# Kernel optimization log

Measured on AMD Instinct MI355X. Metric: run time of the kernel, lower is better.

## Reference

```python
import jax, jax.numpy as jnp
import numpy as np

B, T, C = 4, 2048, 2048
N_HEAD = 16
HEAD_DIM = C // N_HEAD  # 128
ROPE_BASE = 10000.0


def rope_cache(dim, seq_len, base=ROPE_BASE):
    inv_freq = 1.0 / (base ** (jnp.arange(0, dim, 2, dtype=jnp.float32) / dim))
    t = jnp.arange(seq_len, dtype=jnp.float32)
    freqs = jnp.outer(t, inv_freq)  # [T, dim//2]
    return jnp.cos(freqs), jnp.sin(freqs)


def apply_rope(q, k, cos, sin):
    # q, k: [B, H, T, D], interleaved-pair rotation
    q1, q2 = q[..., 0::2], q[..., 1::2]
    k1, k2 = k[..., 0::2], k[..., 1::2]
    c = cos[None, None, :, :]
    s = sin[None, None, :, :]
    q_rot = jnp.stack([q1 * c - q2 * s, q1 * s + q2 * c], axis=-1).reshape(q.shape)
    k_rot = jnp.stack([k1 * c - k2 * s, k1 * s + k2 * c], axis=-1).reshape(k.shape)
    return q_rot, k_rot


def setup_inputs() -> dict:
    key = jax.random.key(0)
    k1, k2, k3 = jax.random.split(key, 3)
    x = jax.random.normal(k1, (B, T, C), dtype=jnp.float32)
    W_attn = jax.random.normal(k2, (3 * C, C), dtype=jnp.float32) * (1.0 / np.sqrt(C))
    W_proj = jax.random.normal(k3, (C, C), dtype=jnp.float32) * (1.0 / np.sqrt(C))
    return {"x": x, "W_attn": W_attn, "W_proj": W_proj}


def reference(x, W_attn, W_proj):
    Bx, Tx, Cx = x.shape
    qkv = jnp.einsum('btc,fc->btf', x, W_attn)  # [B, T, 3C]
    q, k, v = jnp.split(qkv, 3, axis=-1)
    # [B, H, T, D]
    q = q.reshape(Bx, Tx, N_HEAD, HEAD_DIM).transpose(0, 2, 1, 3)
    k = k.reshape(Bx, Tx, N_HEAD, HEAD_DIM).transpose(0, 2, 1, 3)
    v = v.reshape(Bx, Tx, N_HEAD, HEAD_DIM).transpose(0, 2, 1, 3)
    cos, sin = rope_cache(HEAD_DIM, Tx)
    q, k = apply_rope(q, k, cos, sin)
    scale = 1.0 / np.sqrt(HEAD_DIM)
    scores = jnp.einsum('bhqd,bhkd->bhqk', q, k) * scale
    causal = jnp.tril(jnp.ones((Tx, Tx), dtype=bool))
    scores = jnp.where(causal[None, None, :, :], scores, jnp.finfo(scores.dtype).min)
    attn = jax.nn.softmax(scores, axis=-1)
    y = jnp.einsum('bhqk,bhkd->bhqd', attn, v)
    y = y.transpose(0, 2, 1, 3).reshape(Bx, Tx, Cx)
    return jnp.einsum('btc,fc->btf', y, W_proj)
```

## Files before the change

### kernel.cpp

```cpp
#include <hip/hip_runtime.h>
#include <stdint.h>

#define TT 2048
#define CC 2048
#define NHEAD 16
#define HD 128
#define NB 4
#define MTOT (NB*TT)
#define KD 2048
#define NT 32

typedef __attribute__((ext_vector_type(8))) short bf16x8;
typedef __attribute__((ext_vector_type(4))) float f32x4;

__device__ __forceinline__ unsigned short f2bf(float f) {
  unsigned u = __float_as_uint(f);
  u += 0x7FFF + ((u >> 16) & 1);
  return (unsigned short)(u >> 16);
}
__device__ __forceinline__ float bf2f(unsigned short h) {
  return __uint_as_float(((unsigned)h) << 16);
}

__device__ __forceinline__ void gl_lds16(const unsigned short* g, short* l) {
  __builtin_amdgcn_global_load_lds(
      (const __attribute__((address_space(1))) void*)(g),
      (__attribute__((address_space(3))) void*)(l), 16, 0, 0);
}

#define MFMA16(a, b, c) __builtin_amdgcn_mfma_f32_16x16x32_bf16((a), (b), (c), 0, 0, 0)

#define PRE_MFMA() do { \
  __builtin_amdgcn_s_barrier(); \
  asm volatile("s_waitcnt lgkmcnt(0)" ::: "memory"); \
  __builtin_amdgcn_s_setprio(1); \
} while(0)
#define POST_MFMA() do { \
  __builtin_amdgcn_s_setprio(0); \
  __builtin_amdgcn_s_barrier(); \
  __builtin_amdgcn_sched_barrier(0); \
} while(0)

__global__ void k_f2b(const float* __restrict__ in, unsigned short* __restrict__ out, int n4) {
  int i = blockIdx.x * 256 + threadIdx.x;
  if (i >= n4) return;
  float4 v = reinterpret_cast<const float4*>(in)[i];
  ushort4 o;
  o.x = f2bf(v.x); o.y = f2bf(v.y); o.z = f2bf(v.z); o.w = f2bf(v.w);
  reinterpret_cast<ushort4*>(out)[i] = o;
}

__global__ void k_rope_tab(float* __restrict__ tab) {
  int t = blockIdx.x, i = threadIdx.x;
  double inv = exp2(-(double)i * (13.287712379549449062 / 64.0));
  double ang = (double)t * inv;
  tab[(t*64 + i)*2 + 0] = (float)cos(ang);
  tab[(t*64 + i)*2 + 1] = (float)sin(ang);
}

__device__ __forceinline__ void gemm256_core(
    const unsigned short* __restrict__ Ag,
    const unsigned short* __restrict__ Bg,
    int m0, int n0, short* lds, f32x4 (&acc)[8][4])
{
  const int tid = threadIdx.x;
  const int wid = tid >> 6, lane = tid & 63;
  const int wm = wid >> 2, wn = wid & 3;
  const int r15 = lane & 15, hi4 = lane >> 4;
  const int srow = wid*8 + (lane >> 3);
  const int schunk = (lane & 7) ^ (lane >> 3);

  const f32x4 fz = {0.f, 0.f, 0.f, 0.f};
#pragma unroll
  for (int i = 0; i < 8; i++)
#pragma unroll
    for (int j = 0; j < 4; j++) acc[i][j] = fz;

  int aoff0[8];
#pragma unroll
  for (int mi = 0; mi < 8; mi++) {
    int row = wm*128 + mi*16 + r15;
    aoff0[mi] = row*64 + ((hi4 ^ (row & 7))*8);
  }
  int boff0[4];
#pragma unroll
  for (int ni = 0; ni < 4; ni++) {
    int row = wn*64 + ni*16 + r15;
    boff0[ni] = row*64 + ((hi4 ^ (row & 7))*8);
  }

#define STAGE(G, L, GROW0, KT) do { \
    gl_lds16((G) + (size_t)((GROW0) + srow)*KD + (KT) + schunk*8, (L) + wid*512); \
    gl_lds16((G) + (size_t)((GROW0) + 64 + srow)*KD + (KT) + schunk*8, (L) + 4096 + wid*512); \
  } while(0)

  STAGE(Ag, lds,                        m0,       0);
  STAGE(Ag, lds + 8192,                 m0 + 128, 0);
  STAGE(Bg, lds + 32768,                n0,       0);
  STAGE(Bg, lds + 32768 + 8192,         n0 + 128, 0);
  STAGE(Bg, lds + 32768 + 16384,        n0,       64);
  STAGE(Bg, lds + 32768 + 16384 + 8192, n0 + 128, 64);
  asm volatile("s_waitcnt vmcnt(4)" ::: "memory");
  __builtin_amdgcn_s_barrier();
  __builtin_amdgcn_sched_barrier(0);

#pragma unroll 1
  for (int t = 0; t < NT; t++) {
    const int db = t & 1;
    short* Ab = lds + db*16384;
    short* Bb = lds + 32768 + db*16384;
    short* An = lds + (db ^ 1)*16384;
    const int kt = t*64;
    const bool stA = (t < NT - 1);
    const bool stB = (t < NT - 2);

    bf16x8 a[8], b[4][2];
#pragma unroll
    for (int mi = 0; mi < 8; mi++)
      a[mi] = *reinterpret_cast<const bf16x8*>(Ab + aoff0[mi]);
#pragma unroll
    for (int ni = 0; ni < 4; ni++) {
      b[ni][0] = *reinterpret_cast<const bf16x8*>(Bb + boff0[ni]);
      b[ni][1] = *reinterpret_cast<const bf16x8*>(Bb + (boff0[ni] ^ 32));
    }
    if (stA) {
      STAGE(Ag, An,        m0,       kt + 64);
      STAGE(Ag, An + 8192, m0 + 128, kt + 64);
    }
    PRE_MFMA();
#pragma unroll
    for (int mi = 0; mi < 8; mi++)
#pragma unroll
      for (int ni = 0; ni < 4; ni++)
        acc[mi][ni] = MFMA16(a[mi], b[ni][0], acc[mi][ni]);
    POST_MFMA();

#pragma unroll
    for (int mi = 0; mi < 8; mi++)
      a[mi] = *reinterpret_cast<const bf16x8*>(Ab + (aoff0[mi] ^ 32));
    if (stB) {
      STAGE(Bg, Bb,        n0,       kt + 128);
      STAGE(Bg, Bb + 8192, n0 + 128, kt + 128);
    }
    if (t >= NT - 2) asm volatile("s_waitcnt vmcnt(0)" ::: "memory");
    else             asm volatile("s_waitcnt vmcnt(4)" ::: "memory");
    PRE_MFMA();
#pragma unroll
    for (int mi = 0; mi < 8; mi++)
#pragma unroll
      for (int ni = 0; ni < 4; ni++)
        acc[mi][ni] = MFMA16(a[mi], b[ni][1], acc[mi][ni]);
    POST_MFMA();
  }
#undef STAGE
}

__global__ __launch_bounds__(512, 2) void k_qkv(
    const unsigned short* __restrict__ xb,
    const unsigned short* __restrict__ wab,
    unsigned short* __restrict__ qr,
    unsigned short* __restrict__ kr,
    unsigned short* __restrict__ vt)
{
  __shared__ __align__(16) short lds[65536];
  f32x4 acc[8][4];
  int bid = blockIdx.x;
  int swz = (bid & 7)*96 + (bid >> 3);
  int m0 = (swz / 24)*256, n0 = (swz % 24)*256;
  gemm256_core(xb, wab, m0, n0, lds, acc);

  int tid = threadIdx.x, wid = tid >> 6, lane = tid & 63;
  int wm = wid >> 2, wn = wid & 3, r15 = lane & 15, hi4 = lane >> 4;
  int nw0 = n0 + wn*64;
  int which = nw0 >> 11;
  int h = (nw0 & 2047) >> 7;
#pragma unroll
  for (int mi = 0; mi < 8; mi++) {
    int m_base = m0 + wm*128 + mi*16 + hi4*4;
    int b = m_base >> 11;
    int t0 = m_base & (TT - 1);
#pragma unroll
    for (int ni = 0; ni < 4; ni++) {
      int d = (nw0 & 127) + ni*16 + r15;
      if (which == 2) {
        ushort4 pv;
        pv.x = f2bf(acc[mi][ni][0]); pv.y = f2bf(acc[mi][ni][1]);
        pv.z = f2bf(acc[mi][ni][2]); pv.w = f2bf(acc[mi][ni][3]);
        *reinterpret_cast<ushort4*>(vt + ((size_t)((b*NHEAD + h)*HD + d))*TT + t0) = pv;
      } else {
        unsigned short* dst = (which == 0) ? qr : kr;
        size_t base = ((size_t)(b*NHEAD + h)*TT + t0)*HD + d;
#pragma unroll
        for (int r = 0; r < 4; r++) dst[base + (size_t)r*HD] = f2bf(acc[mi][ni][r]);
      }
    }
  }
}

__global__ __launch_bounds__(512, 2) void k_proj(
    const unsigned short* __restrict__ yb,
    const unsigned short* __restrict__ wpb,
    float* __restrict__ out)
{
  __shared__ __align__(16) short lds[65536];
  f32x4 acc[8][4];
  int bid = blockIdx.x;
  int swz = (bid & 7)*32 + (bid >> 3);
  int m0 = (swz / 8)*256, n0 = (swz % 8)*256;
  gemm256_core(yb, wpb, m0, n0, lds, acc);

  int tid = threadIdx.x, wid = tid >> 6, lane = tid & 63;
  int wm = wid >> 2, wn = wid & 3, r15 = lane & 15, hi4 = lane >> 4;
  int nw0 = n0 + wn*64;
#pragma unroll
  for (int mi = 0; mi < 8; mi++) {
    int m = m0 + wm*128 + mi*16 + hi4*4;
#pragma unroll
    for (int ni = 0; ni < 4; ni++) {
      int n = nw0 + ni*16 + r15;
#pragma unroll
      for (int r = 0; r < 4; r++)
        out[(size_t)(m + r)*CC + n] = acc[mi][ni][r];
    }
  }
}

__global__ void k_rope_apply(unsigned int* __restrict__ q32, unsigned int* __restrict__ k32,
                             const float* __restrict__ tab) {
  int i = blockIdx.x * 256 + threadIdx.x;
  int ii = i & 63;
  int t = (i >> 6) & (TT - 1);
  float c = tab[(t*64 + ii)*2], s = tab[(t*64 + ii)*2 + 1];
  unsigned qv = q32[i];
  float q1 = bf2f((unsigned short)qv), q2 = bf2f((unsigned short)(qv >> 16));
  unsigned short lo = f2bf(q1*c - q2*s), hi = f2bf(q1*s + q2*c);
  q32[i] = (unsigned)lo | ((unsigned)hi << 16);
  unsigned kv = k32[i];
  float k1 = bf2f((unsigned short)kv), k2 = bf2f((unsigned short)(kv >> 16));
  lo = f2bf(k1*c - k2*s); hi = f2bf(k1*s + k2*c);
  k32[i] = (unsigned)lo | ((unsigned)hi << 16);
}

__global__ __launch_bounds__(256) void k_attn(
    const unsigned short* __restrict__ qr,
    const unsigned short* __restrict__ kr,
    const unsigned short* __restrict__ vt,
    unsigned short* __restrict__ yb)
{
  __shared__ short Ks[64*128];
  __shared__ short Vs[128*64];
  __shared__ short Pw[4*16*64];
  int bid = blockIdx.x;
  int bh = bid & 63, pr = bid >> 6;
  int tid = threadIdx.x, w = tid >> 6, lane = tid & 63;
  int r15 = lane & 15, hi4 = lane >> 4;
  const unsigned short* qg = qr + (size_t)bh*TT*HD;
  const unsigned short* kg = kr + (size_t)bh*TT*HD;
  const unsigned short* vg = vt + (size_t)bh*HD*TT;
  const f32x4 fz = {0.f,0.f,0.f,0.f};
  const float scale = 0.08838834764831845f;
  int b = bh >> 4, h = bh & 15;

#pragma unroll 1
  for (int ph = 0; ph < 2; ph++) {
    int qb = ph ? (31 - pr) : pr;
    int qlo = qb*64 + w*16;
    bf16x8 qf[4];
    {
      int qrow = qlo + r15;
#pragma unroll
      for (int kk = 0; kk < 4; kk++)
        qf[kk] = *reinterpret_cast<const bf16x8*>(qg + (size_t)qrow*HD + kk*32 + hi4*8);
    }
    f32x4 ao[8];
#pragma unroll
    for (int i = 0; i < 8; i++) ao[i] = fz;
    float mrow[4], lsum[4];
#pragma unroll
    for (int r = 0; r < 4; r++) { mrow[r] = -3.0e38f; lsum[r] = 0.f; }
    int ntiles = qb + 1;
    for (int it = 0; it < ntiles; ++it) {
      int kv0 = it*64;
      __syncthreads();
#pragma unroll
      for (int i = 0; i < 4; i++) {
        int chunk = tid + i*256;
        int row = chunk >> 4, c16 = chunk & 15;
        uint4 v = *reinterpret_cast<const uint4*>(kg + (size_t)(kv0 + row)*HD + c16*8);
        *reinterpret_cast<uint4*>((char*)Ks + row*256 + ((c16 ^ (row & 7))*16)) = v;
      }
#pragma unroll
      for (int i = 0; i < 4; i++) {
        int chunk = tid + i*256;
        int d = chunk >> 3, c8 = chunk & 7;
        uint4 v = *reinterpret_cast<const uint4*>(vg + (size_t)d*TT + kv0 + c8*8);
        *reinterpret_cast<uint4*>((char*)Vs + d*128 + ((c8 ^ (d & 7))*16)) = v;
      }
      __syncthreads();
      f32x4 sacc[4];
#pragma unroll
      for (int n = 0; n < 4; n++) {
        sacc[n] = fz;
#pragma unroll
        for (int kk = 0; kk < 4; kk++) {
          int kvr = n*16 + r15;
          int ch = (kk*4 + hi4) ^ (kvr & 7);
          bf16x8 kf = *reinterpret_cast<const bf16x8*>((char*)Ks + kvr*256 + ch*16);
          sacc[n] = MFMA16(qf[kk], kf, sacc[n]);
        }
      }
      float p[4][4], rmax[4];
#pragma unroll
      for (int r = 0; r < 4; r++) {
        int qgi = qlo + hi4*4 + r;
        float mx = -3.0e38f;
#pragma unroll
        for (int n = 0; n < 4; n++) {
          int kvg = kv0 + n*16 + r15;
          float sv = sacc[n][r]*scale;
          sv = (kvg <= qgi) ? sv : -3.0e38f;
          p[n][r] = sv;
          mx = fmaxf(mx, sv);
        }
        rmax[r] = mx;
      }
#pragma unroll
      for (int mm = 1; mm < 16; mm <<= 1)
#pragma unroll
        for (int r = 0; r < 4; r++) rmax[r] = fmaxf(rmax[r], __shfl_xor(rmax[r], mm));
      float alpha[4], rsum[4];
#pragma unroll
      for (int r = 0; r < 4; r++) {
        float mnew = fmaxf(mrow[r], rmax[r]);
        alpha[r] = __expf(mrow[r] - mnew);
        mrow[r] = mnew;
        float sum = 0.f;
#pragma unroll
        for (int n = 0; n < 4; n++) {
          float pv = __expf(p[n][r] - mnew);
          p[n][r] = pv;
          sum += pv;
        }
        rsum[r] = sum;
      }
#pragma unroll
      for (int mm = 1; mm < 16; mm <<= 1)
#pragma unroll
        for (int r = 0; r < 4; r++) rsum[r] += __shfl_xor(rsum[r], mm);
#pragma unroll
      for (int r = 0; r < 4; r++) lsum[r] = lsum[r]*alpha[r] + rsum[r];
#pragma unroll
      for (int i = 0; i < 8; i++)
#pragma unroll
        for (int r = 0; r < 4; r++) ao[i][r] *= alpha[r];
#pragma unroll
      for (int r = 0; r < 4; r++) {
        int prow = hi4*4 + r;
#pragma unroll
        for (int n = 0; n < 4; n++) {
          int col = n*16 + r15;
          Pw[w*1024 + prow*64 + (col ^ ((prow & 7) << 3))] = (short)f2bf(p[n][r]);
        }
      }
#pragma unroll
      for (int kk = 0; kk < 2; kk++) {
        int prow = r15;
        int ch = (kk*4 + hi4) ^ (prow & 7);
        bf16x8 pa = *reinterpret_cast<const bf16x8*>((char*)(Pw + w*1024) + prow*128 + ch*16);
#pragma unroll
        for (int ds_ = 0; ds_ < 8; ds_++) {
          int d = ds_*16 + r15;
          int vch = (kk*4 + hi4) ^ (d & 7);
          bf16x8 vf = *reinterpret_cast<const bf16x8*>((char*)Vs + d*128 + vch*16);
          ao[ds_] = MFMA16(pa, vf, ao[ds_]);
        }
      }
    }
#pragma unroll
    for (int r = 0; r < 4; r++) {
      int t = qlo + hi4*4 + r;
      float inv = 1.f / lsum[r];
      size_t base = ((size_t)b*TT + t)*CC + h*HD + r15;
#pragma unroll
      for (int ds_ = 0; ds_ < 8; ds_++)
        yb[base + ds_*16] = f2bf(ao[ds_][r] * inv);
    }
  }
}

extern "C" void kernel_launch(void* const* d_in, const int* in_sizes, int n_in,
                              void* d_out, int out_size, void* d_ws, size_t ws_size,
                              hipStream_t stream) {
  const float* x  = (const float*)d_in[0];
  const float* wa = (const float*)d_in[1];
  const float* wp = (const float*)d_in[2];
  float* out = (float*)d_out;
  char* ws = (char*)d_ws;
  size_t off = 0;
  unsigned short* xb  = (unsigned short*)(ws + off); off += (size_t)MTOT*CC*2;
  unsigned short* wab = (unsigned short*)(ws + off); off += (size_t)3*CC*CC*2;
  unsigned short* wpb = (unsigned short*)(ws + off); off += (size_t)CC*CC*2;
  unsigned short* qr  = (unsigned short*)(ws + off); off += (size_t)MTOT*CC*2;
  unsigned short* kr  = (unsigned short*)(ws + off); off += (size_t)MTOT*CC*2;
  unsigned short* vt  = (unsigned short*)(ws + off); off += (size_t)MTOT*CC*2;
  unsigned short* yb  = (unsigned short*)(ws + off); off += (size_t)MTOT*CC*2;
  float* tab          = (float*)(ws + off);          off += (size_t)TT*64*2*4;

  k_f2b<<<dim3(16384), dim3(256), 0, stream>>>(x,  xb,  MTOT*CC/4);
  k_f2b<<<dim3(12288), dim3(256), 0, stream>>>(wa, wab, 3*CC*CC/4);
  k_f2b<<<dim3(4096),  dim3(256), 0, stream>>>(wp, wpb, CC*CC/4);
  k_rope_tab<<<dim3(TT), dim3(64), 0, stream>>>(tab);
  k_qkv<<<dim3(768), dim3(512), 0, stream>>>(xb, wab, qr, kr, vt);
  k_rope_apply<<<dim3(32768), dim3(256), 0, stream>>>((unsigned int*)qr, (unsigned int*)kr, tab);
  k_attn<<<dim3(1024), dim3(256), 0, stream>>>(qr, kr, vt, yb);
  k_proj<<<dim3(256), dim3(512), 0, stream>>>(yb, wpb, out);
}
```

Before: 494.6 us.

## Process two 64-row query blocks per wave with prefetched K/V and lazy rescaling

The attention kernel now gives each block 128 query rows, with each wave holding two 16-row Q fragments. Each K/V tile loaded into LDS is reused across twice as many queries, and the grid is halved. The next K/V tile is prefetched into registers while the current tile is computed, and the online softmax skips the accumulator rescale when no row max grows by more than 8. This cuts global K/V traffic and barriers per query, at the cost of more registers, lower occupancy and coarser causal load balancing.

```diff
diff --git a/kernel.cpp b/kernel.cpp
--- a/kernel.cpp
+++ b/kernel.cpp
@@ -249,7 +249,7 @@
 {
   __shared__ short Ks[64*128];
   __shared__ short Vs[128*64];
-  __shared__ short Pw[4*16*64];
+  __shared__ short Pw[4*32*64];
   int bid = blockIdx.x;
   int bh = bid & 63, pr = bid >> 6;
   int tid = threadIdx.x, w = tid >> 6, lane = tid & 63;
@@ -261,129 +261,251 @@
   const float scale = 0.08838834764831845f;
   int b = bh >> 4, h = bh & 15;
 
+  int kdst[4], vdst[4], ksoff[4];
+  size_t vsoff[4];
+#pragma unroll
+  for (int i = 0; i < 4; i++) {
+    int chunk = tid + i*256;
+    int row = chunk >> 4, c16 = chunk & 15;
+    kdst[i] = row*256 + ((c16 ^ (row & 7))*16);
+    ksoff[i] = row*HD + c16*8;
+    int d = chunk >> 3, c8 = chunk & 7;
+    vdst[i] = d*128 + ((c8 ^ (d & 7))*16);
+    vsoff[i] = (size_t)d*TT + c8*8;
+  }
+
 #pragma unroll 1
   for (int ph = 0; ph < 2; ph++) {
-    int qb = ph ? (31 - pr) : pr;
-    int qlo = qb*64 + w*16;
-    bf16x8 qf[4];
+    int qb = ph ? (15 - pr) : pr;
+    int qlo0 = qb*128 + w*16, qlo1 = qlo0 + 64;
+    bf16x8 qf0[4], qf1[4];
     {
-      int qrow = qlo + r15;
-#pragma unroll
-      for (int kk = 0; kk < 4; kk++)
-        qf[kk] = *reinterpret_cast<const bf16x8*>(qg + (size_t)qrow*HD + kk*32 + hi4*8);
-    }
-    f32x4 ao[8];
-#pragma unroll
-    for (int i = 0; i < 8; i++) ao[i] = fz;
-    float mrow[4], lsum[4];
-#pragma unroll
-    for (int r = 0; r < 4; r++) { mrow[r] = -3.0e38f; lsum[r] = 0.f; }
-    int ntiles = qb + 1;
+      int q0 = qlo0 + r15, q1 = qlo1 + r15;
+#pragma unroll
+      for (int kk = 0; kk < 4; kk++) {
+        qf0[kk] = *reinterpret_cast<const bf16x8*>(qg + (size_t)q0*HD + kk*32 + hi4*8);
+        qf1[kk] = *reinterpret_cast<const bf16x8*>(qg + (size_t)q1*HD + kk*32 + hi4*8);
+      }
+    }
+    f32x4 ao0[8], ao1[8];
+#pragma unroll
+    for (int i = 0; i < 8; i++) { ao0[i] = fz; ao1[i] = fz; }
+    float mrow0[4], lsum0[4], mrow1[4], lsum1[4];
+#pragma unroll
+    for (int r = 0; r < 4; r++) {
+      mrow0[r] = -3.0e38f; lsum0[r] = 0.f;
+      mrow1[r] = -3.0e38f; lsum1[r] = 0.f;
+    }
+    int ntiles = 2*qb + 2;
+    uint4 st[8];
+
+#pragma unroll
+    for (int i = 0; i < 4; i++) {
+      st[i]     = *reinterpret_cast<const uint4*>(kg + ksoff[i]);
+      st[4 + i] = *reinterpret_cast<const uint4*>(vg + vsoff[i]);
+    }
+    __syncthreads();
+#pragma unroll
+    for (int i = 0; i < 4; i++) {
+      *reinterpret_cast<uint4*>((char*)Ks + kdst[i]) = st[i];
+      *reinterpret_cast<uint4*>((char*)Vs + vdst[i]) = st[4 + i];
+    }
+    __syncthreads();
+
+#pragma unroll 1
     for (int it = 0; it < ntiles; ++it) {
       int kv0 = it*64;
-      __syncthreads();
-#pragma unroll
-      for (int i = 0; i < 4; i++) {
-        int chunk = tid + i*256;
-        int row = chunk >> 4, c16 = chunk & 15;
-        uint4 v = *reinterpret_cast<const uint4*>(kg + (size_t)(kv0 + row)*HD + c16*8);
-        *reinterpret_cast<uint4*>((char*)Ks + row*256 + ((c16 ^ (row & 7))*16)) = v;
-      }
-#pragma unroll
-      for (int i = 0; i < 4; i++) {
-        int chunk = tid + i*256;
-        int d = chunk >> 3, c8 = chunk & 7;
-        uint4 v = *reinterpret_cast<const uint4*>(vg + (size_t)d*TT + kv0 + c8*8);
-        *reinterpret_cast<uint4*>((char*)Vs + d*128 + ((c8 ^ (d & 7))*16)) = v;
-      }
-      __syncthreads();
-      f32x4 sacc[4];
+      bool more = (it + 1 < ntiles);
+      f32x4 s0[4], s1[4];
 #pragma unroll
       for (int n = 0; n < 4; n++) {
-        sacc[n] = fz;
+        s0[n] = fz; s1[n] = fz;
 #pragma unroll
         for (int kk = 0; kk < 4; kk++) {
           int kvr = n*16 + r15;
           int ch = (kk*4 + hi4) ^ (kvr & 7);
           bf16x8 kf = *reinterpret_cast<const bf16x8*>((char*)Ks + kvr*256 + ch*16);
-          sacc[n] = MFMA16(qf[kk], kf, sacc[n]);
-        }
-      }
-      float p[4][4], rmax[4];
-#pragma unroll
-      for (int r = 0; r < 4; r++) {
-        int qgi = qlo + hi4*4 + r;
-        float mx = -3.0e38f;
-#pragma unroll
-        for (int n = 0; n < 4; n++) {
-          int kvg = kv0 + n*16 + r15;
-          float sv = sacc[n][r]*scale;
-          sv = (kvg <= qgi) ? sv : -3.0e38f;
-          p[n][r] = sv;
-          mx = fmaxf(mx, sv);
-        }
-        rmax[r] = mx;
-      }
-#pragma unroll
-      for (int mm = 1; mm < 16; mm <<= 1)
-#pragma unroll
-        for (int r = 0; r < 4; r++) rmax[r] = fmaxf(rmax[r], __shfl_xor(rmax[r], mm));
-      float alpha[4], rsum[4];
-#pragma unroll
-      for (int r = 0; r < 4; r++) {
-        float mnew = fmaxf(mrow[r], rmax[r]);
-        alpha[r] = __expf(mrow[r] - mnew);
-        mrow[r] = mnew;
-        float sum = 0.f;
-#pragma unroll
-        for (int n = 0; n < 4; n++) {
-          float pv = __expf(p[n][r] - mnew);
-          p[n][r] = pv;
-          sum += pv;
-        }
-        rsum[r] = sum;
-      }
-#pragma unroll
-      for (int mm = 1; mm < 16; mm <<= 1)
-#pragma unroll
-        for (int r = 0; r < 4; r++) rsum[r] += __shfl_xor(rsum[r], mm);
-#pragma unroll
-      for (int r = 0; r < 4; r++) lsum[r] = lsum[r]*alpha[r] + rsum[r];
-#pragma unroll
-      for (int i = 0; i < 8; i++)
-#pragma unroll
-        for (int r = 0; r < 4; r++) ao[i][r] *= alpha[r];
-#pragma unroll
-      for (int r = 0; r < 4; r++) {
-        int prow = hi4*4 + r;
-#pragma unroll
-        for (int n = 0; n < 4; n++) {
-          int col = n*16 + r15;
-          Pw[w*1024 + prow*64 + (col ^ ((prow & 7) << 3))] = (short)f2bf(p[n][r]);
+          s1[n] = MFMA16(qf1[kk], kf, s1[n]);
+          s0[n] = MFMA16(qf0[kk], kf, s0[n]);
+        }
+      }
+      if (more) {
+        int nkv = kv0 + 64;
+#pragma unroll
+        for (int i = 0; i < 4; i++) {
+          st[i]     = *reinterpret_cast<const uint4*>(kg + (size_t)nkv*HD + ksoff[i]);
+          st[4 + i] = *reinterpret_cast<const uint4*>(vg + vsoff[i] + nkv);
+        }
+      }
+      {
+        float p[4][4], rmax[4];
+#pragma unroll
+        for (int r = 0; r < 4; r++) {
+          int qgi = qlo0 + hi4*4 + r;
+          float mx = -3.0e38f;
+#pragma unroll
+          for (int n = 0; n < 4; n++) {
+            int kvg = kv0 + n*16 + r15;
+            float sv = s0[n][r]*scale;
+            sv = (kvg <= qgi) ? sv : -3.0e38f;
+            p[n][r] = sv;
+            mx = fmaxf(mx, sv);
+          }
+          rmax[r] = mx;
+        }
+#pragma unroll
+        for (int mm = 1; mm < 16; mm <<= 1)
+#pragma unroll
+          for (int r = 0; r < 4; r++) rmax[r] = fmaxf(rmax[r], __shfl_xor(rmax[r], mm));
+        bool ng = (rmax[0] <= mrow0[0] + 8.f) && (rmax[1] <= mrow0[1] + 8.f)
+               && (rmax[2] <= mrow0[2] + 8.f) && (rmax[3] <= mrow0[3] + 8.f);
+        bool defer = __all(ng);
+        float alpha[4];
+#pragma unroll
+        for (int r = 0; r < 4; r++) {
+          if (defer) { alpha[r] = 1.f; }
+          else {
+            float mnew = fmaxf(mrow0[r], rmax[r]);
+            alpha[r] = __expf(mrow0[r] - mnew);
+            mrow0[r] = mnew;
+          }
+        }
+        float rsum[4];
+#pragma unroll
+        for (int r = 0; r < 4; r++) {
+          float sum = 0.f;
+#pragma unroll
+          for (int n = 0; n < 4; n++) {
+            float pv = __expf(p[n][r] - mrow0[r]);
+            p[n][r] = pv; sum += pv;
+          }
+          rsum[r] = sum;
+        }
+#pragma unroll
+        for (int mm = 1; mm < 16; mm <<= 1)
+#pragma unroll
+          for (int r = 0; r < 4; r++) rsum[r] += __shfl_xor(rsum[r], mm);
+#pragma unroll
+        for (int r = 0; r < 4; r++) lsum0[r] = lsum0[r]*alpha[r] + rsum[r];
+        if (!defer) {
+#pragma unroll
+          for (int i = 0; i < 8; i++)
+#pragma unroll
+            for (int r = 0; r < 4; r++) ao0[i][r] *= alpha[r];
+        }
+#pragma unroll
+        for (int r = 0; r < 4; r++) {
+          int prow = hi4*4 + r;
+#pragma unroll
+          for (int n = 0; n < 4; n++) {
+            int col = n*16 + r15;
+            Pw[w*2048 + prow*64 + (col ^ ((prow & 7) << 3))] = (short)f2bf(p[n][r]);
+          }
+        }
+      }
+      {
+        float p[4][4], rmax[4];
+#pragma unroll
+        for (int r = 0; r < 4; r++) {
+          int qgi = qlo1 + hi4*4 + r;
+          float mx = -3.0e38f;
+#pragma unroll
+          for (int n = 0; n < 4; n++) {
+            int kvg = kv0 + n*16 + r15;
+            float sv = s1[n][r]*scale;
+            sv = (kvg <= qgi) ? sv : -3.0e38f;
+            p[n][r] = sv;
+            mx = fmaxf(mx, sv);
+          }
+          rmax[r] = mx;
+        }
+#pragma unroll
+        for (int mm = 1; mm < 16; mm <<= 1)
+#pragma unroll
+          for (int r = 0; r < 4; r++) rmax[r] = fmaxf(rmax[r], __shfl_xor(rmax[r], mm));
+        bool ng = (rmax[0] <= mrow1[0] + 8.f) && (rmax[1] <= mrow1[1] + 8.f)
+               && (rmax[2] <= mrow1[2] + 8.f) && (rmax[3] <= mrow1[3] + 8.f);
+        bool defer = __all(ng);
+        float alpha[4];
+#pragma unroll
+        for (int r = 0; r < 4; r++) {
+          if (defer) { alpha[r] = 1.f; }
+          else {
+            float mnew = fmaxf(mrow1[r], rmax[r]);
+            alpha[r] = __expf(mrow1[r] - mnew);
+            mrow1[r] = mnew;
+          }
+        }
+        float rsum[4];
+#pragma unroll
+        for (int r = 0; r < 4; r++) {
+          float sum = 0.f;
+#pragma unroll
+          for (int n = 0; n < 4; n++) {
+            float pv = __expf(p[n][r] - mrow1[r]);
+            p[n][r] = pv; sum += pv;
+          }
+          rsum[r] = sum;
+        }
+#pragma unroll
+        for (int mm = 1; mm < 16; mm <<= 1)
+#pragma unroll
+          for (int r = 0; r < 4; r++) rsum[r] += __shfl_xor(rsum[r], mm);
+#pragma unroll
+        for (int r = 0; r < 4; r++) lsum1[r] = lsum1[r]*alpha[r] + rsum[r];
+        if (!defer) {
+#pragma unroll
+          for (int i = 0; i < 8; i++)
+#pragma unroll
+            for (int r = 0; r < 4; r++) ao1[i][r] *= alpha[r];
+        }
+#pragma unroll
+        for (int r = 0; r < 4; r++) {
+          int prow = 16 + hi4*4 + r;
+#pragma unroll
+          for (int n = 0; n < 4; n++) {
+            int col = n*16 + r15;
+            Pw[w*2048 + prow*64 + (col ^ ((prow & 7) << 3))] = (short)f2bf(p[n][r]);
+          }
         }
       }
 #pragma unroll
       for (int kk = 0; kk < 2; kk++) {
-        int prow = r15;
-        int ch = (kk*4 + hi4) ^ (prow & 7);
-        bf16x8 pa = *reinterpret_cast<const bf16x8*>((char*)(Pw + w*1024) + prow*128 + ch*16);
+        int ch = (kk*4 + hi4) ^ (r15 & 7);
+        bf16x8 pa0 = *reinterpret_cast<const bf16x8*>((char*)Pw + w*4096 + r15*128 + ch*16);
+        bf16x8 pa1 = *reinterpret_cast<const bf16x8*>((char*)Pw + w*4096 + (16 + r15)*128 + ch*16);
 #pragma unroll
         for (int ds_ = 0; ds_ < 8; ds_++) {
           int d = ds_*16 + r15;
           int vch = (kk*4 + hi4) ^ (d & 7);
           bf16x8 vf = *reinterpret_cast<const bf16x8*>((char*)Vs + d*128 + vch*16);
-          ao[ds_] = MFMA16(pa, vf, ao[ds_]);
-        }
+          ao1[ds_] = MFMA16(pa1, vf, ao1[ds_]);
+          ao0[ds_] = MFMA16(pa0, vf, ao0[ds_]);
+        }
+      }
+      if (more) {
+        __syncthreads();
+#pragma unroll
+        for (int i = 0; i < 4; i++) {
+          *reinterpret_cast<uint4*>((char*)Ks + kdst[i]) = st[i];
+          *reinterpret_cast<uint4*>((char*)Vs + vdst[i]) = st[4 + i];
+        }
+        __syncthreads();
       }
     }
 #pragma unroll
     for (int r = 0; r < 4; r++) {
-      int t = qlo + hi4*4 + r;
-      float inv = 1.f / lsum[r];
-      size_t base = ((size_t)b*TT + t)*CC + h*HD + r15;
-#pragma unroll
-      for (int ds_ = 0; ds_ < 8; ds_++)
-        yb[base + ds_*16] = f2bf(ao[ds_][r] * inv);
+      int t0 = qlo0 + hi4*4 + r;
+      int t1 = qlo1 + hi4*4 + r;
+      float inv0 = 1.f / lsum0[r];
+      float inv1 = 1.f / lsum1[r];
+      size_t base0 = ((size_t)b*TT + t0)*CC + h*HD + r15;
+      size_t base1 = ((size_t)b*TT + t1)*CC + h*HD + r15;
+#pragma unroll
+      for (int ds_ = 0; ds_ < 8; ds_++) {
+        yb[base0 + ds_*16] = f2bf(ao0[ds_][r] * inv0);
+        yb[base1 + ds_*16] = f2bf(ao1[ds_][r] * inv1);
+      }
     }
   }
 }
@@ -412,6 +534,6 @@
   k_rope_tab<<<dim3(TT), dim3(64), 0, stream>>>(tab);
   k_qkv<<<dim3(768), dim3(512), 0, stream>>>(xb, wab, qr, kr, vt);
   k_rope_apply<<<dim3(32768), dim3(256), 0, stream>>>((unsigned int*)qr, (unsigned int*)kr, tab);
-  k_attn<<<dim3(1024), dim3(256), 0, stream>>>(qr, kr, vt, yb);
+  k_attn<<<dim3(512), dim3(256), 0, stream>>>(qr, kr, vt, yb);
   k_proj<<<dim3(256), dim3(512), 0, stream>>>(yb, wpb, out);
 }
```

New measurement: 733.9 us. 1.48x slower.

## Rewrite attention with 32x32 MFMA, double-buffered async KV loads, lazy rescale

Applied to the files above, without the earlier changes.

The attention kernel now has each block cover a 128-query tile (32 rows per wave) and uses 32x32x16 bf16 MFMAs with S computed transposed (K as the A operand), so P can be turned into the PV operand through lane shuffles instead of an LDS round trip. K/V tiles are double-buffered in LDS and filled with global_load_lds, which overlaps the next tile's loads with the current tile's compute. Other changes: masking is skipped on fully visible tiles, the online-softmax rescale is deferred while the running max moves by 8 or less, bf16 packing uses v_cvt_pk, and MFMA sections raise wave priority. The grid is halved and launch bounds pin occupancy, which trades parallelism and latency hiding for a larger register tile.

```diff
diff --git a/kernel.cpp b/kernel.cpp
--- a/kernel.cpp
+++ b/kernel.cpp
@@ -12,6 +12,8 @@
 
 typedef __attribute__((ext_vector_type(8))) short bf16x8;
 typedef __attribute__((ext_vector_type(4))) float f32x4;
+typedef __attribute__((ext_vector_type(16))) float f32x16;
+typedef __attribute__((ext_vector_type(4))) unsigned u32x4;
 
 __device__ __forceinline__ unsigned short f2bf(float f) {
   unsigned u = __float_as_uint(f);
@@ -29,6 +31,7 @@
 }
 
 #define MFMA16(a, b, c) __builtin_amdgcn_mfma_f32_16x16x32_bf16((a), (b), (c), 0, 0, 0)
+#define MFMA32(a, b, c) __builtin_amdgcn_mfma_f32_32x32x16_bf16((a), (b), (c), 0, 0, 0)
 
 #define PRE_MFMA() do { \
   __builtin_amdgcn_s_barrier(); \
@@ -241,151 +244,185 @@
   k32[i] = (unsigned)lo | ((unsigned)hi << 16);
 }
 
-__global__ __launch_bounds__(256) void k_attn(
+__global__ __launch_bounds__(256, 1) void k_attn(
     const unsigned short* __restrict__ qr,
     const unsigned short* __restrict__ kr,
     const unsigned short* __restrict__ vt,
     unsigned short* __restrict__ yb)
 {
-  __shared__ short Ks[64*128];
-  __shared__ short Vs[128*64];
-  __shared__ short Pw[4*16*64];
+  __shared__ __align__(16) short Ks[2][64*128];
+  __shared__ __align__(16) short Vs[2][128*64];
+  __shared__ float alds[4][32];
   int bid = blockIdx.x;
   int bh = bid & 63, pr = bid >> 6;
   int tid = threadIdx.x, w = tid >> 6, lane = tid & 63;
-  int r15 = lane & 15, hi4 = lane >> 4;
+  int l31 = lane & 31, hi = lane >> 5;
   const unsigned short* qg = qr + (size_t)bh*TT*HD;
   const unsigned short* kg = kr + (size_t)bh*TT*HD;
   const unsigned short* vg = vt + (size_t)bh*HD*TT;
-  const f32x4 fz = {0.f,0.f,0.f,0.f};
   const float scale = 0.08838834764831845f;
   int b = bh >> 4, h = bh & 15;
 
+  int ksoff[4], vsoff[4];
+#pragma unroll
+  for (int i = 0; i < 4; i++) {
+    int rK = (w*4 + i)*4 + (lane >> 4);
+    int cK = (lane & 15) ^ (rK & 7);
+    ksoff[i] = rK*HD + cK*8;
+    int dV = (w*4 + i)*8 + (lane >> 3);
+    int cV = (lane & 7) ^ (dV & 7);
+    vsoff[i] = dV*TT + cV*8;
+  }
+
+#define STAGE_KV(BUF, KV0) do { \
+    _Pragma("unroll") \
+    for (int i_ = 0; i_ < 4; i_++) { \
+      gl_lds16(kg + (size_t)(KV0)*HD + ksoff[i_], &Ks[BUF][(w*4 + i_)*512]); \
+      gl_lds16(vg + (KV0) + vsoff[i_],            &Vs[BUF][(w*4 + i_)*512]); \
+    } \
+  } while(0)
+
 #pragma unroll 1
   for (int ph = 0; ph < 2; ph++) {
-    int qb = ph ? (31 - pr) : pr;
-    int qlo = qb*64 + w*16;
-    bf16x8 qf[4];
-    {
-      int qrow = qlo + r15;
-#pragma unroll
-      for (int kk = 0; kk < 4; kk++)
-        qf[kk] = *reinterpret_cast<const bf16x8*>(qg + (size_t)qrow*HD + kk*32 + hi4*8);
-    }
-    f32x4 ao[8];
-#pragma unroll
-    for (int i = 0; i < 8; i++) ao[i] = fz;
-    float mrow[4], lsum[4];
-#pragma unroll
-    for (int r = 0; r < 4; r++) { mrow[r] = -3.0e38f; lsum[r] = 0.f; }
-    int ntiles = qb + 1;
+    int qb = ph ? (15 - pr) : pr;
+    int qlo = qb*128 + w*32;
+    int qgi = qlo + l31;
+    bf16x8 qf[8];
+#pragma unroll
+    for (int kk = 0; kk < 8; kk++)
+      qf[kk] = *reinterpret_cast<const bf16x8*>(qg + (size_t)qgi*HD + kk*16 + hi*8);
+
+    f32x16 ao[4];
+#pragma unroll
+    for (int dt = 0; dt < 4; dt++)
+#pragma unroll
+      for (int r = 0; r < 16; r++) ao[dt][r] = 0.f;
+    float mrow = -3.0e38f, lsum = 0.f;
+    int ntiles = 2*qb + 2;
+
+    STAGE_KV(0, 0);
+    __syncthreads();
+    int cur = 0;
+
+#pragma unroll 1
     for (int it = 0; it < ntiles; ++it) {
       int kv0 = it*64;
-      __syncthreads();
-#pragma unroll
-      for (int i = 0; i < 4; i++) {
-        int chunk = tid + i*256;
-        int row = chunk >> 4, c16 = chunk & 15;
-        uint4 v = *reinterpret_cast<const uint4*>(kg + (size_t)(kv0 + row)*HD + c16*8);
-        *reinterpret_cast<uint4*>((char*)Ks + row*256 + ((c16 ^ (row & 7))*16)) = v;
-      }
-#pragma unroll
-      for (int i = 0; i < 4; i++) {
-        int chunk = tid + i*256;
-        int d = chunk >> 3, c8 = chunk & 7;
-        uint4 v = *reinterpret_cast<const uint4*>(vg + (size_t)d*TT + kv0 + c8*8);
-        *reinterpret_cast<uint4*>((char*)Vs + d*128 + ((c8 ^ (d & 7))*16)) = v;
+      if (it + 1 < ntiles) STAGE_KV(cur ^ 1, kv0 + 64);
+      if (kv0 <= qlo + 31) {
+        const short* Kc = Ks[cur];
+        const short* Vc = Vs[cur];
+        bool full = (kv0 + 63 <= qlo);
+        f32x16 s0, s1;
+#pragma unroll
+        for (int r = 0; r < 16; r++) { s0[r] = 0.f; s1[r] = 0.f; }
+        __builtin_amdgcn_s_setprio(1);
+#pragma unroll
+        for (int kk = 0; kk < 8; kk++) {
+          int row0 = l31, row1 = 32 + l31;
+          int ch0 = ((2*kk + hi) ^ (row0 & 7));
+          int ch1 = ((2*kk + hi) ^ (row1 & 7));
+          bf16x8 kf0 = *reinterpret_cast<const bf16x8*>((const char*)Kc + row0*256 + ch0*16);
+          bf16x8 kf1 = *reinterpret_cast<const bf16x8*>((const char*)Kc + row1*256 + ch1*16);
+          s0 = MFMA32(kf0, qf[kk], s0);
+          s1 = MFMA32(kf1, qf[kk], s1);
+        }
+        __builtin_amdgcn_s_setprio(0);
+        float p[32];
+#pragma unroll
+        for (int r = 0; r < 16; r++) {
+          int kvl = (r & 3) + 8*(r >> 2) + 4*hi;
+          float v0 = s0[r]*scale, v1 = s1[r]*scale;
+          if (!full) {
+            v0 = (kv0 + kvl      <= qgi) ? v0 : -3.0e38f;
+            v1 = (kv0 + 32 + kvl <= qgi) ? v1 : -3.0e38f;
+          }
+          p[r] = v0; p[16 + r] = v1;
+        }
+        float t16[16];
+#pragma unroll
+        for (int i = 0; i < 16; i++) t16[i] = fmaxf(p[i], p[i + 16]);
+#pragma unroll
+        for (int i = 0; i < 8; i++) t16[i] = fmaxf(t16[i], t16[i + 8]);
+#pragma unroll
+        for (int i = 0; i < 4; i++) t16[i] = fmaxf(t16[i], t16[i + 4]);
+        float mx = fmaxf(fmaxf(t16[0], t16[1]), fmaxf(t16[2], t16[3]));
+        mx = fmaxf(mx, __shfl_xor(mx, 32));
+        bool defer = __all(mx <= mrow + 8.f);
+        if (!defer) {
+          float mnew = fmaxf(mrow, mx);
+          float alpha = __expf(mrow - mnew);
+          mrow = mnew;
+          lsum *= alpha;
+          if (lane < 32) alds[w][lane] = alpha;
+#pragma unroll
+          for (int r = 0; r < 16; r++) {
+            int ql = (r & 3) + 8*(r >> 2) + 4*hi;
+            float av = alds[w][ql];
+#pragma unroll
+            for (int dt = 0; dt < 4; dt++) ao[dt][r] *= av;
+          }
+        }
+#pragma unroll
+        for (int i = 0; i < 32; i++) p[i] = __expf(p[i] - mrow);
+#pragma unroll
+        for (int i = 0; i < 16; i++) t16[i] = p[i] + p[i + 16];
+#pragma unroll
+        for (int i = 0; i < 8; i++) t16[i] = t16[i] + t16[i + 8];
+#pragma unroll
+        for (int i = 0; i < 4; i++) t16[i] = t16[i] + t16[i + 4];
+        float rs = (t16[0] + t16[1]) + (t16[2] + t16[3]);
+        rs += __shfl_xor(rs, 32);
+        lsum += rs;
+        bf16x8 pa[4];
+#pragma unroll
+        for (int ks = 0; ks < 4; ks++) {
+          const int base = (ks >> 1)*16 + (ks & 1)*8;
+          unsigned a0, a1, b0, b1;
+          asm("v_cvt_pk_bf16_f32 %0, %1, %2" : "=v"(a0) : "v"(p[base + 0]), "v"(p[base + 1]));
+          asm("v_cvt_pk_bf16_f32 %0, %1, %2" : "=v"(a1) : "v"(p[base + 2]), "v"(p[base + 3]));
+          asm("v_cvt_pk_bf16_f32 %0, %1, %2" : "=v"(b0) : "v"(p[base + 4]), "v"(p[base + 5]));
+          asm("v_cvt_pk_bf16_f32 %0, %1, %2" : "=v"(b1) : "v"(p[base + 6]), "v"(p[base + 7]));
+          unsigned sa0 = (unsigned)__shfl_xor((int)a0, 32);
+          unsigned sa1 = (unsigned)__shfl_xor((int)a1, 32);
+          unsigned sb0 = (unsigned)__shfl_xor((int)b0, 32);
+          unsigned sb1 = (unsigned)__shfl_xor((int)b1, 32);
+          u32x4 pw;
+          pw.x = hi ? sb0 : a0;
+          pw.y = hi ? sb1 : a1;
+          pw.z = hi ? b0 : sa0;
+          pw.w = hi ? b1 : sa1;
+          pa[ks] = __builtin_bit_cast(bf16x8, pw);
+        }
+        __builtin_amdgcn_s_setprio(1);
+#pragma unroll
+        for (int dt = 0; dt < 4; dt++) {
+          int d = dt*32 + l31;
+#pragma unroll
+          for (int ks = 0; ks < 4; ks++) {
+            int ch = ((2*ks + hi) ^ (d & 7));
+            bf16x8 vf = *reinterpret_cast<const bf16x8*>((const char*)Vc + d*128 + ch*16);
+            ao[dt] = MFMA32(pa[ks], vf, ao[dt]);
+          }
+        }
+        __builtin_amdgcn_s_setprio(0);
       }
       __syncthreads();
-      f32x4 sacc[4];
-#pragma unroll
-      for (int n = 0; n < 4; n++) {
-        sacc[n] = fz;
-#pragma unroll
-        for (int kk = 0; kk < 4; kk++) {
-          int kvr = n*16 + r15;
-          int ch = (kk*4 + hi4) ^ (kvr & 7);
-          bf16x8 kf = *reinterpret_cast<const bf16x8*>((char*)Ks + kvr*256 + ch*16);
-          sacc[n] = MFMA16(qf[kk], kf, sacc[n]);
-        }
-      }
-      float p[4][4], rmax[4];
-#pragma unroll
-      for (int r = 0; r < 4; r++) {
-        int qgi = qlo + hi4*4 + r;
-        float mx = -3.0e38f;
-#pragma unroll
-        for (int n = 0; n < 4; n++) {
-          int kvg = kv0 + n*16 + r15;
-          float sv = sacc[n][r]*scale;
-          sv = (kvg <= qgi) ? sv : -3.0e38f;
-          p[n][r] = sv;
-          mx = fmaxf(mx, sv);
-        }
-        rmax[r] = mx;
-      }
-#pragma unroll
-      for (int mm = 1; mm < 16; mm <<= 1)
-#pragma unroll
-        for (int r = 0; r < 4; r++) rmax[r] = fmaxf(rmax[r], __shfl_xor(rmax[r], mm));
-      float alpha[4], rsum[4];
-#pragma unroll
-      for (int r = 0; r < 4; r++) {
-        float mnew = fmaxf(mrow[r], rmax[r]);
-        alpha[r] = __expf(mrow[r] - mnew);
-        mrow[r] = mnew;
-        float sum = 0.f;
-#pragma unroll
-        for (int n = 0; n < 4; n++) {
-          float pv = __expf(p[n][r] - mnew);
-          p[n][r] = pv;
-          sum += pv;
-        }
-        rsum[r] = sum;
-      }
-#pragma unroll
-      for (int mm = 1; mm < 16; mm <<= 1)
-#pragma unroll
-        for (int r = 0; r < 4; r++) rsum[r] += __shfl_xor(rsum[r], mm);
-#pragma unroll
-      for (int r = 0; r < 4; r++) lsum[r] = lsum[r]*alpha[r] + rsum[r];
-#pragma unroll
-      for (int i = 0; i < 8; i++)
-#pragma unroll
-        for (int r = 0; r < 4; r++) ao[i][r] *= alpha[r];
-#pragma unroll
-      for (int r = 0; r < 4; r++) {
-        int prow = hi4*4 + r;
-#pragma unroll
-        for (int n = 0; n < 4; n++) {
-          int col = n*16 + r15;
-          Pw[w*1024 + prow*64 + (col ^ ((prow & 7) << 3))] = (short)f2bf(p[n][r]);
-        }
-      }
-#pragma unroll
-      for (int kk = 0; kk < 2; kk++) {
-        int prow = r15;
-        int ch = (kk*4 + hi4) ^ (prow & 7);
-        bf16x8 pa = *reinterpret_cast<const bf16x8*>((char*)(Pw + w*1024) + prow*128 + ch*16);
-#pragma unroll
-        for (int ds_ = 0; ds_ < 8; ds_++) {
-          int d = ds_*16 + r15;
-          int vch = (kk*4 + hi4) ^ (d & 7);
-          bf16x8 vf = *reinterpret_cast<const bf16x8*>((char*)Vs + d*128 + vch*16);
-          ao[ds_] = MFMA16(pa, vf, ao[ds_]);
-        }
-      }
-    }
-#pragma unroll
-    for (int r = 0; r < 4; r++) {
-      int t = qlo + hi4*4 + r;
-      float inv = 1.f / lsum[r];
-      size_t base = ((size_t)b*TT + t)*CC + h*HD + r15;
-#pragma unroll
-      for (int ds_ = 0; ds_ < 8; ds_++)
-        yb[base + ds_*16] = f2bf(ao[ds_][r] * inv);
-    }
-  }
+      cur ^= 1;
+    }
+    if (lane < 32) alds[w][lane] = 1.0f / lsum;
+#pragma unroll
+    for (int r = 0; r < 16; r++) {
+      int ql = (r & 3) + 8*(r >> 2) + 4*hi;
+      float lv = alds[w][ql];
+      int t = qlo + ql;
+      size_t base = ((size_t)b*TT + t)*CC + h*HD + l31;
+#pragma unroll
+      for (int dt = 0; dt < 4; dt++)
+        yb[base + dt*32] = f2bf(ao[dt][r] * lv);
+    }
+    __syncthreads();
+  }
+#undef STAGE_KV
 }
 
 extern "C" void kernel_launch(void* const* d_in, const int* in_sizes, int n_in,
@@ -412,6 +449,6 @@
   k_rope_tab<<<dim3(TT), dim3(64), 0, stream>>>(tab);
   k_qkv<<<dim3(768), dim3(512), 0, stream>>>(xb, wab, qr, kr, vt);
   k_rope_apply<<<dim3(32768), dim3(256), 0, stream>>>((unsigned int*)qr, (unsigned int*)kr, tab);
-  k_attn<<<dim3(1024), dim3(256), 0, stream>>>(qr, kr, vt, yb);
+  k_attn<<<dim3(512), dim3(256), 0, stream>>>(qr, kr, vt, yb);
   k_proj<<<dim3(256), dim3(512), 0, stream>>>(yb, wpb, out);
 }
```

After: 485.5 us. About the same (-1.8%).
